# Kernel optimization log

Measured on AMD Instinct MI355X. Metric: run time of the kernel, lower is better.

Reference implementation:

```python
import jax, jax.numpy as jnp
import numpy as np

B, N, H = 16, 1024, 1024


def setup_inputs() -> dict:
    key = jax.random.key(0)
    ks = jax.random.split(key, 12)
    inv = 1.0 / np.sqrt(H)
    inp = {
        "x": jax.random.normal(ks[0], (B, N, H), jnp.float32),
        "atom_graph": jax.random.normal(ks[1], (B, N, N), jnp.float32),
        "variable_graph": jax.random.normal(ks[2], (B, N, N), jnp.float32),
        "Wq": jax.random.uniform(ks[3], (H, H), jnp.float32, -inv, inv),
        "bq": jax.random.uniform(ks[4], (H,), jnp.float32, -inv, inv),
        "Wk": jax.random.uniform(ks[5], (H, H), jnp.float32, -inv, inv),
        "bk": jax.random.uniform(ks[6], (H,), jnp.float32, -inv, inv),
        "Wv": jax.random.uniform(ks[7], (H, H), jnp.float32, -inv, inv),
        "bv": jax.random.uniform(ks[8], (H,), jnp.float32, -inv, inv),
        "predicate_pos": jax.random.randint(ks[9], (B, N), 0, 2, jnp.int32),
        "variable_tags": jax.random.randint(ks[10], (B, N), 0, 4, jnp.int32),
    }
    return inp


def _path_pool(h, predicate_pos):
    # h: [B,N,H]; predicate_pos: [B,N] in {0,1}
    b, n, d = h.shape
    i = jnp.arange(n)
    # pos[i-2] (value irrelevant for i<2, those branches handled explicitly)
    pp2 = jnp.pad(predicate_pos, ((0, 0), (2, 0)))[:, :n]  # [B,N]
    # window [s, e): i==0 -> [0,2); i==1 -> [0,3); pos[i-2]==1 -> [i,i+2); else [i-1,i+2)
    s = jnp.where(i < 2, 0, jnp.where(pp2 == 1, i, i - 1))  # [B,N]
    e = jnp.where(i == 0, 2, jnp.where(i == 1, 3, i + 2))    # [N]
    e = jnp.minimum(e, n)
    e = jnp.broadcast_to(e, (b, n))
    # prefix sums along node dim with a leading zero row -> windowed means via gather
    cs = jnp.concatenate([jnp.zeros((b, 1, d), h.dtype), jnp.cumsum(h, axis=1)], axis=1)  # [B,N+1,H]
    win_sum = (jnp.take_along_axis(cs, e[:, :, None], axis=1)
               - jnp.take_along_axis(cs, s[:, :, None], axis=1))  # [B,N,H]
    means = win_sum / (e - s)[:, :, None].astype(h.dtype)
    mask = (predicate_pos == 1).astype(h.dtype)  # [B,N]
    item = (means * mask[:, :, None]).sum(axis=1) / mask.sum(axis=1)[:, None]  # [B,H]
    return jnp.broadcast_to(item[:, None, :], (b, n, d))


def reference(x, atom_graph, variable_graph, Wq, bq, Wk, bk, Wv, bv,
              predicate_pos, variable_tags):
    scale = x.shape[-1] ** (-0.5)
    q = (x @ Wq.T + bq) * scale
    k = x @ Wk.T + bk
    v = x @ Wv.T + bv
    att = jnp.einsum("bnh,bmh->bnm", q, k) + atom_graph + variable_graph
    att = jax.nn.softmax(att, axis=-1)  # dropout is identity in eval
    h = jnp.einsum("bnm,bmh->bnh", att, v)
    return _path_pool(h, predicate_pos)
```

## Files before the change

### kernel.cpp

```cpp
#include <hip/hip_runtime.h>
#include <hip/hip_bf16.h>

#define BATCH 16
#define SEQ   1024
#define DIM   1024

typedef __attribute__((ext_vector_type(8))) short bf16x8;
typedef __attribute__((ext_vector_type(4))) float f32x4;
typedef __attribute__((ext_vector_type(4))) unsigned short us4;

__device__ __forceinline__ float bfu2f(unsigned short u) {
  union { unsigned int i; float f; } c; c.i = ((unsigned int)u) << 16; return c.f;
}
__device__ __forceinline__ unsigned short f2bfu(float f) {
  union { float f; unsigned int i; } c; c.f = f;
  return (unsigned short)((c.i + 0x7FFFu + ((c.i >> 16) & 1u)) >> 16);
}
__device__ __forceinline__ void async16(void* lds, const void* g) {
  __builtin_amdgcn_global_load_lds(
      (const __attribute__((address_space(1))) unsigned int*)g,
      (__attribute__((address_space(3))) unsigned int*)lds, 16, 0, 0);
}

__global__ void cast_xw_kernel(const float* __restrict__ x, const float* __restrict__ Wv,
                               unsigned short* __restrict__ xb,
                               unsigned short* __restrict__ Wvb, int x4) {
  int i = blockIdx.x * blockDim.x + threadIdx.x;
  const float* in; unsigned short* out; int j;
  if (i < x4) { in = x; out = xb; j = i; }
  else { in = Wv; out = Wvb; j = i - x4; }
  f32x4 v = ((const f32x4*)in)[j];
  us4 o;
  o[0] = f2bfu(v[0]); o[1] = f2bfu(v[1]); o[2] = f2bfu(v[2]); o[3] = f2bfu(v[3]);
  ((us4*)out)[j] = o;
}

__global__ void castT_kernel(const float* __restrict__ Wq, const float* __restrict__ Wk,
                             unsigned short* __restrict__ WqT,
                             unsigned short* __restrict__ WkT) {
  const float* in = (blockIdx.z == 0) ? Wq : Wk;
  unsigned short* out = (blockIdx.z == 0) ? WqT : WkT;
  __shared__ float t[64][65];
  const int h0 = blockIdx.x * 64, i0 = blockIdx.y * 64;
  const int tid = threadIdx.x;
  const int sub = tid >> 4, c4 = tid & 15;
#pragma unroll
  for (int p = 0; p < 4; ++p) {
    const int row = p * 16 + sub;
    f32x4 v = *(const f32x4*)(in + (size_t)(h0 + row) * DIM + i0 + c4 * 4);
    t[row][c4 * 4 + 0] = v[0]; t[row][c4 * 4 + 1] = v[1];
    t[row][c4 * 4 + 2] = v[2]; t[row][c4 * 4 + 3] = v[3];
  }
  __syncthreads();
#pragma unroll
  for (int p = 0; p < 4; ++p) {
    const int orow = p * 16 + sub;
    us4 o;
    o[0] = f2bfu(t[c4 * 4 + 0][orow]);
    o[1] = f2bfu(t[c4 * 4 + 1][orow]);
    o[2] = f2bfu(t[c4 * 4 + 2][orow]);
    o[3] = f2bfu(t[c4 * 4 + 3][orow]);
    *(us4*)(out + (size_t)(i0 + orow) * DIM + h0 + c4 * 4) = o;
  }
}

__global__ void t12_kernel(const unsigned short* __restrict__ WqT,
                           const unsigned short* __restrict__ WkT,
                           const float* __restrict__ bq, const float* __restrict__ bk,
                           float* __restrict__ t1, float* __restrict__ t2) {
  const int y = blockIdx.y;
  const unsigned short* Wt = y ? WkT : WqT;
  const float* vec = y ? bq : bk;
  float* tout = y ? t2 : t1;
  const int wave = threadIdx.x >> 6, lane = threadIdx.x & 63;
  const int i = blockIdx.x * 4 + wave;
  const us4* wr = (const us4*)(Wt + (size_t)i * DIM);
  float s = 0.f;
#pragma unroll
  for (int t = 0; t < 4; ++t) {
    us4 w4 = wr[lane + 64 * t];
    f32x4 b4 = *(const f32x4*)(vec + (lane + 64 * t) * 4);
    s += bfu2f(w4[0]) * b4[0] + bfu2f(w4[1]) * b4[1] +
         bfu2f(w4[2]) * b4[2] + bfu2f(w4[3]) * b4[3];
  }
#pragma unroll
  for (int o = 32; o; o >>= 1) s += __shfl_down(s, o);
  if (lane == 0) tout[i] = s;
}

__global__ void ac_kernel(const unsigned short* __restrict__ xb,
                          const float* __restrict__ t1, const float* __restrict__ t2,
                          const float* __restrict__ bq, const float* __restrict__ bk,
                          float* __restrict__ a, float* __restrict__ c) {
  const float scale = 0.03125f;
  const int tid = threadIdx.x;
  const int wave = tid >> 6, lane = tid & 63;
  float dp = 0.f;
  for (int i = tid; i < DIM; i += 256) dp += bq[i] * bk[i];
#pragma unroll
  for (int o = 32; o; o >>= 1) dp += __shfl_down(dp, o);
  __shared__ float dred[4];
  if ((tid & 63) == 0) dred[tid >> 6] = dp;
  __syncthreads();
  const float d = dred[0] + dred[1] + dred[2] + dred[3];
  float t1r[16], t2r[16];
#pragma unroll
  for (int t = 0; t < 4; ++t) {
    f32x4 v1 = *(const f32x4*)(t1 + (lane + 64 * t) * 4);
    f32x4 v2 = *(const f32x4*)(t2 + (lane + 64 * t) * 4);
#pragma unroll
    for (int j = 0; j < 4; ++j) { t1r[t * 4 + j] = v1[j]; t2r[t * 4 + j] = v2[j]; }
  }
  for (int rr = 0; rr < 16; ++rr) {
    const int row = blockIdx.x * 64 + wave * 16 + rr;
    const us4* xr = (const us4*)(xb + (size_t)row * DIM);
    float sa = 0.f, sc = 0.f;
#pragma unroll
    for (int t = 0; t < 4; ++t) {
      us4 v = xr[lane + 64 * t];
#pragma unroll
      for (int j = 0; j < 4; ++j) {
        const float f = bfu2f(v[j]);
        sa += f * t1r[t * 4 + j];
        sc += f * t2r[t * 4 + j];
      }
    }
#pragma unroll
    for (int o = 32; o; o >>= 1) { sa += __shfl_down(sa, o); sc += __shfl_down(sc, o); }
    if (lane == 0) {
      a[row] = scale * (sa + d);
      c[row] = scale * sc;
    }
  }
}

__global__ void pathw_kernel(const int* __restrict__ pos, float* __restrict__ w,
                             float* __restrict__ zbias) {
  const int b = blockIdx.x;
  __shared__ int ps[SEQ];
  __shared__ int mcnt;
  const int tid = threadIdx.x;
  if (tid == 0) mcnt = 0;
  __syncthreads();
  if (b == 0)
    for (int i = tid; i < DIM; i += 256) zbias[i] = 0.f;
  for (int i = tid; i < SEQ; i += 256) ps[i] = pos[b * SEQ + i];
  __syncthreads();
  int c = 0;
  for (int i = tid; i < SEQ; i += 256) c += ps[i];
  for (int o = 32; o; o >>= 1) c += __shfl_down(c, o);
  if ((tid & 63) == 0) atomicAdd(&mcnt, c);
  __syncthreads();
  const float invM = 1.0f / (float)mcnt;
  for (int j = tid; j < SEQ; j += 256) {
    float a = 0.f;
#pragma unroll
    for (int di = -1; di <= 1; ++di) {
      int i = j + di;
      if (i < 0 || i >= SEQ) continue;
      if (!ps[i]) continue;
      int s, e;
      if (i < 2) { s = 0; e = (i == 0) ? 2 : 3; }
      else { s = (ps[i - 2] == 1) ? i : (i - 1); e = i + 2; if (e > SEQ) e = SEQ; }
      if (s <= j && j < e) a += 1.0f / (float)(e - s);
    }
    w[b * SEQ + j] = a * invM;
  }
}

__global__ void proj_gemm(const unsigned short* __restrict__ A,
                          const unsigned short* __restrict__ W,
                          const float* __restrict__ bias, float alpha,
                          unsigned short* __restrict__ C, int M, int N, int K)
{
  __shared__ __align__(16) char smem[32768];
  float* Sl = (float*)smem;
  const int tid = threadIdx.x;
  const int wave = tid >> 6, lane = tid & 63;
  const int lr = lane & 15, lg = lane >> 4;
  const int wr = wave >> 1, wc = wave & 1;
  const int m0 = blockIdx.x * 128, n0 = blockIdx.y * 128;
  const int off0 = tid * 16, off1 = 4096 + tid * 16;
  const int r0 = off0 >> 6, ke0 = (off0 >> 1) & 31;
  const int r1 = off1 >> 6, ke1 = (off1 >> 1) & 31;
  f32x4 acc[4][4] = {};

  auto stage = [&](char* base, int kk) {
    async16(base + off0, A + (size_t)(m0 + r0) * K + kk + ke0);
    async16(base + off1, A + (size_t)(m0 + r1) * K + kk + ke1);
    async16(base + 8192 + off0, W + (size_t)(n0 + r0) * K + kk + ke0);
    async16(base + 8192 + off1, W + (size_t)(n0 + r1) * K + kk + ke1);
  };
  auto compute = [&](const char* base) {
    bf16x8 af[4], bfv[4];
#pragma unroll
    for (int i = 0; i < 4; ++i) {
      af[i]  = *(const bf16x8*)(base + ((wr * 64 + i * 16 + lr) << 6) + (lg << 4));
      bfv[i] = *(const bf16x8*)(base + 8192 + ((wc * 64 + i * 16 + lr) << 6) + (lg << 4));
    }
#pragma unroll
    for (int i = 0; i < 4; ++i)
#pragma unroll
      for (int j = 0; j < 4; ++j)
        acc[i][j] = __builtin_amdgcn_mfma_f32_16x16x32_bf16(af[i], bfv[j], acc[i][j], 0, 0, 0);
  };

  const int nt = K >> 5;
  stage(smem, 0);
  __syncthreads();
  int cur = 0;
  for (int k = 0; k < nt - 1; ++k) {
    stage(smem + ((cur ^ 1) << 14), (k + 1) << 5);
    compute(smem + (cur << 14));
    __syncthreads();
    cur ^= 1;
  }
  compute(smem + (cur << 14));
#pragma unroll
  for (int p = 0; p < 4; ++p) {
    __syncthreads();
    if (wr == (p >> 1)) {
      const int ibase = (p & 1) * 2;
#pragma unroll
      for (int ii = 0; ii < 2; ++ii) {
        const int i = ibase + ii;
#pragma unroll
        for (int j = 0; j < 4; ++j)
#pragma unroll
          for (int r = 0; r < 4; ++r)
            Sl[(ii * 16 + lg * 4 + r) * 132 + wc * 64 + j * 16 + lr] = acc[i][j][r];
      }
    }
    __syncthreads();
#pragma unroll
    for (int it = 0; it < 4; ++it) {
      const int v = tid + it * 256;
      const int lrow = v >> 5, c4 = v & 31;
      const int grow = m0 + p * 32 + lrow;
      const int col = n0 + c4 * 4;
      const f32x4 s4 = *(const f32x4*)(&Sl[lrow * 132 + c4 * 4]);
      const f32x4 b4 = *(const f32x4*)(bias + col);
      us4 o;
      o[0] = f2bfu((s4[0] + b4[0]) * alpha);
      o[1] = f2bfu((s4[1] + b4[1]) * alpha);
      o[2] = f2bfu((s4[2] + b4[2]) * alpha);
      o[3] = f2bfu((s4[3] + b4[3]) * alpha);
      *(us4*)(C + (size_t)grow * N + col) = o;
    }
  }
}

__global__ __launch_bounds__(512, 2)
void gemm256(const unsigned short* __restrict__ A,
             const unsigned short* __restrict__ B,
             unsigned short* __restrict__ C)
{
  extern __shared__ __align__(16) char smem[];
  const size_t boff = (size_t)blockIdx.z << 20;
  const int m0 = blockIdx.y * 256, n0 = blockIdx.x * 256;
  const int tid = threadIdx.x;
  const int lane = tid & 63;
  const int wid = tid >> 6;
  const int wm = wid >> 2, wn = wid & 3;
  const int lr = lane & 15, lg = lane >> 4;
  const unsigned short* Ab = A + boff;
  const unsigned short* Bb = B + boff;

  int sr[2], se[2], sL[2];
#pragma unroll
  for (int l = 0; l < 2; ++l) {
    const int L = l * 8192 + tid * 16;
    const int r = L >> 6, sp = (L >> 4) & 3;
    sL[l] = L; sr[l] = r; se[l] = (sp ^ ((r >> 1) & 3)) * 8;
  }
  int aoff[8], boff_[4];
#pragma unroll
  for (int i = 0; i < 8; ++i) {
    const int row = wm * 128 + i * 16 + lr;
    aoff[i] = row * 64 + (lg ^ ((row >> 1) & 3)) * 16;
  }
#pragma unroll
  for (int j = 0; j < 4; ++j) {
    const int row = wn * 64 + j * 16 + lr;
    boff_[j] = row * 64 + (lg ^ ((row >> 1) & 3)) * 16;
  }

  auto stage = [&](int slot, int kt) {
    char* sa = smem + slot * 32768;
#pragma unroll
    for (int l = 0; l < 2; ++l)
      async16(sa + sL[l], Ab + (size_t)(m0 + sr[l]) * DIM + kt * 32 + se[l]);
    char* sb = sa + 16384;
#pragma unroll
    for (int l = 0; l < 2; ++l)
      async16(sb + sL[l], Bb + (size_t)(n0 + sr[l]) * DIM + kt * 32 + se[l]);
  };

  f32x4 acc[8][4] = {};
  stage(0, 0); stage(1, 1); stage(2, 2); stage(3, 3);

#pragma unroll
  for (int t = 0; t < 32; ++t) {
    const int rem = 31 - t;
    if (rem >= 3)      asm volatile("s_waitcnt vmcnt(12)" ::: "memory");
    else if (rem == 2) asm volatile("s_waitcnt vmcnt(8)" ::: "memory");
    else if (rem == 1) asm volatile("s_waitcnt vmcnt(4)" ::: "memory");
    else               asm volatile("s_waitcnt vmcnt(0)" ::: "memory");
    __builtin_amdgcn_s_barrier();
    const char* sa = smem + (t & 3) * 32768;
    const char* sb = sa + 16384;
    bf16x8 a[8], bfr[4];
#pragma unroll
    for (int i = 0; i < 8; ++i) a[i] = *(const bf16x8*)(sa + aoff[i]);
#pragma unroll
    for (int j = 0; j < 4; ++j) bfr[j] = *(const bf16x8*)(sb + boff_[j]);
    __builtin_amdgcn_s_setprio(1);
#pragma unroll
    for (int i = 0; i < 8; ++i)
#pragma unroll
      for (int j = 0; j < 4; ++j)
        acc[i][j] = __builtin_amdgcn_mfma_f32_16x16x32_bf16(a[i], bfr[j], acc[i][j], 0, 0, 0);
    __builtin_amdgcn_s_setprio(0);
    __builtin_amdgcn_s_barrier();
    if (t + 4 < 32) stage(t & 3, t + 4);
  }

  unsigned short* Sl = (unsigned short*)smem;
  unsigned short* Cb = C + boff;
#pragma unroll
  for (int half = 0; half < 2; ++half) {
    __syncthreads();
    if (wm == half) {
#pragma unroll
      for (int i = 0; i < 8; ++i)
#pragma unroll
        for (int j = 0; j < 4; ++j)
#pragma unroll
          for (int r = 0; r < 4; ++r)
            Sl[(i * 16 + lg * 4 + r) * 260 + wn * 64 + j * 16 + lr] =
                f2bfu(acc[i][j][r]);
    }
    __syncthreads();
#pragma unroll
    for (int it = 0; it < 16; ++it) {
      const int v = tid + it * 512;
      const int row = v >> 6, c4 = v & 63;
      *(us4*)(Cb + (size_t)(m0 + half * 128 + row) * SEQ + n0 + c4 * 4) =
          *(const us4*)(&Sl[row * 260 + c4 * 4]);
    }
  }
}

__global__ void exp_fused_kernel(const unsigned short* __restrict__ S,
                                 const float* __restrict__ ag, const float* __restrict__ vg,
                                 const float* __restrict__ av, const float* __restrict__ cv,
                                 const float* __restrict__ w, float* __restrict__ part)
{
  __shared__ float red[4][SEQ];
  const int b = blockIdx.y;
  const int tid = threadIdx.x;
  const int wave = tid >> 6, lane = tid & 63;
  const float* agb = ag + ((size_t)b << 20);
  const float* vgb = vg + ((size_t)b << 20);
  const unsigned short* Sb = S + ((size_t)b << 20);
  const float* cvb = cv + b * SEQ;
  f32x4 cq[4];
#pragma unroll
  for (int qi = 0; qi < 4; ++qi)
    cq[qi] = *(const f32x4*)(cvb + (lane + 64 * qi) * 4);
  f32x4 ur[4] = {};
  const int r0 = blockIdx.x * 8 + wave * 2;
#pragma unroll
  for (int r = 0; r < 2; ++r) {
    const int row = r0 + r;
    const float wrow = w[b * SEQ + row];
    if (wrow == 0.f) continue;
    const float arow = av[b * SEQ + row];
    us4 sv[4]; f32x4 a4[4], g4[4];
#pragma unroll
    for (int qi = 0; qi < 4; ++qi) {
      const size_t base = (size_t)row * SEQ + (lane + 64 * qi) * 4;
      sv[qi] = *(const us4*)(Sb + base);
      a4[qi] = *(const f32x4*)(agb + base);
      g4[qi] = *(const f32x4*)(vgb + base);
    }
    float e[16];
    float rs = 0.f;
#pragma unroll
    for (int qi = 0; qi < 4; ++qi)
#pragma unroll
      for (int j = 0; j < 4; ++j) {
        const float ev = __expf(bfu2f(sv[qi][j]) + a4[qi][j] + g4[qi][j] + arow + cq[qi][j]);
        e[qi * 4 + j] = ev;
        rs += ev;
      }
#pragma unroll
    for (int o2 = 32; o2; o2 >>= 1) rs += __shfl_xor(rs, o2);
    const float cn = wrow / rs;
#pragma unroll
    for (int qi = 0; qi < 4; ++qi)
#pragma unroll
      for (int j = 0; j < 4; ++j)
        ur[qi][j] += cn * e[qi * 4 + j];
  }
#pragma unroll
  for (int qi = 0; qi < 4; ++qi)
    *(f32x4*)(&red[wave][(lane + 64 * qi) * 4]) = ur[qi];
  __syncthreads();
  const int col = tid * 4;
  f32x4 s0 = *(const f32x4*)(&red[0][col]);
  const f32x4 s1 = *(const f32x4*)(&red[1][col]);
  const f32x4 s2 = *(const f32x4*)(&red[2][col]);
  const f32x4 s3 = *(const f32x4*)(&red[3][col]);
  s0[0] += s1[0] + s2[0] + s3[0];
  s0[1] += s1[1] + s2[1] + s3[1];
  s0[2] += s1[2] + s2[2] + s3[2];
  s0[3] += s1[3] + s2[3] + s3[3];
  *(f32x4*)(part + ((size_t)(b * 128 + blockIdx.x) << 10) + col) = s0;
}

__global__ void wcol_kernel(const unsigned short* __restrict__ Mt,
                            const float* __restrict__ wv,
                            float* __restrict__ part) {
  const int nc = blockIdx.x;
  const int b = blockIdx.y;
  const int tid = threadIdx.x;
  __shared__ float c[64];
  if (tid < 64) c[tid] = wv[b * SEQ + nc * 64 + tid];
  __syncthreads();
  const unsigned short* p = Mt + ((size_t)b << 20) + ((size_t)(nc * 64) << 10) + tid * 4;
  f32x4 acc = {0.f, 0.f, 0.f, 0.f};
#pragma unroll 8
  for (int n = 0; n < 64; ++n) {
    const us4 v = *(const us4*)(p + ((size_t)n << 10));
    const float cn = c[n];
    acc[0] += cn * bfu2f(v[0]); acc[1] += cn * bfu2f(v[1]);
    acc[2] += cn * bfu2f(v[2]); acc[3] += cn * bfu2f(v[3]);
  }
  *(f32x4*)(part + (size_t)((b * 16 + nc) << 10) + tid * 4) = acc;
}

__global__ void wred_kernel(const float* __restrict__ part, float* __restrict__ vec,
                            int nchunks) {
  const int b = blockIdx.x;
  const int tid = threadIdx.x;
  f32x4 s = {0.f, 0.f, 0.f, 0.f};
  for (int nc = 0; nc < nchunks; ++nc) {
    const f32x4 v = *(const f32x4*)(part + ((size_t)(b * nchunks + nc) << 10) + tid * 4);
    s[0] += v[0]; s[1] += v[1]; s[2] += v[2]; s[3] += v[3];
  }
  *(f32x4*)(vec + b * SEQ + tid * 4) = s;
}

__global__ void item_kernel(const float* __restrict__ y,
                            const unsigned short* __restrict__ Wvb,
                            const float* __restrict__ bv, float* __restrict__ item) {
  const int b = blockIdx.x;
  const int hblk = blockIdx.y;
  __shared__ float ys[DIM];
  const int tid = threadIdx.x;
  for (int i = tid; i < DIM; i += 256) ys[i] = y[b * DIM + i];
  __syncthreads();
  const int wave = tid >> 6, lane = tid & 63;
  const int h = hblk * 4 + wave;
  const us4* wrow = (const us4*)(Wvb + (size_t)h * DIM);
  float acc = 0.f;
#pragma unroll
  for (int t = 0; t < 4; ++t) {
    us4 v = wrow[t * 64 + lane];
    const int d0 = (t * 64 + lane) * 4;
    acc += ys[d0] * bfu2f(v[0]) + ys[d0 + 1] * bfu2f(v[1]) +
           ys[d0 + 2] * bfu2f(v[2]) + ys[d0 + 3] * bfu2f(v[3]);
  }
  for (int o = 32; o; o >>= 1) acc += __shfl_down(acc, o);
  if (lane == 0) item[b * DIM + h] = acc + bv[h];
}

__global__ void bcast_kernel(const float* __restrict__ item, float* __restrict__ out) {
  const int b = blockIdx.y;
  const int n = blockIdx.x;
  const f32x4* src = (const f32x4*)(item + b * DIM);
  f32x4* dst = (f32x4*)(out + (((size_t)b * SEQ + n) << 10));
  dst[threadIdx.x] = src[threadIdx.x];
}

extern "C" void kernel_launch(void* const* d_in, const int* in_sizes, int n_in,
                              void* d_out, int out_size, void* d_ws, size_t ws_size,
                              hipStream_t stream) {
  const float* x    = (const float*)d_in[0];
  const float* ag   = (const float*)d_in[1];
  const float* vgr  = (const float*)d_in[2];
  const float* Wq   = (const float*)d_in[3];
  const float* bq   = (const float*)d_in[4];
  const float* Wk   = (const float*)d_in[5];
  const float* bk   = (const float*)d_in[6];
  const float* Wv   = (const float*)d_in[7];
  const float* bv   = (const float*)d_in[8];
  const int*   pos  = (const int*)d_in[9];
  float* out = (float*)d_out;

  char* ws = (char*)d_ws;
  size_t off = 0;
  auto alloc = [&](size_t bytes) { void* p = ws + off; off += (bytes + 255) & ~(size_t)255; return p; };
  const size_t BNH = (size_t)BATCH * SEQ * DIM;
  unsigned short* xb   = (unsigned short*)alloc(BNH * 2);
  unsigned short* zb   = (unsigned short*)alloc(BNH * 2);
  unsigned short* S    = (unsigned short*)alloc(BNH * 2);
  unsigned short* WqT  = (unsigned short*)alloc((size_t)DIM * DIM * 2);
  unsigned short* WkT  = (unsigned short*)alloc((size_t)DIM * DIM * 2);
  unsigned short* Wvb  = (unsigned short*)alloc((size_t)DIM * DIM * 2);
  unsigned short* Hb   = (unsigned short*)alloc((size_t)DIM * DIM * 2);
  float* w     = (float*)alloc((size_t)BATCH * SEQ * 4);
  float* u     = (float*)alloc((size_t)BATCH * SEQ * 4);
  float* av    = (float*)alloc((size_t)BATCH * SEQ * 4);
  float* cvv   = (float*)alloc((size_t)BATCH * SEQ * 4);
  float* t1    = (float*)alloc((size_t)DIM * 4);
  float* t2    = (float*)alloc((size_t)DIM * 4);
  float* zbias = (float*)alloc((size_t)DIM * 4);
  float* y     = (float*)alloc((size_t)BATCH * DIM * 4);
  float* item  = (float*)alloc((size_t)BATCH * DIM * 4);
  float* part  = (float*)alloc((size_t)BATCH * 128 * SEQ * 4);

  const float scale = 0.03125f;
  const int x4 = (int)(BNH / 4);

  (void)hipFuncSetAttribute(reinterpret_cast<const void*>(gemm256),
                            hipFuncAttributeMaxDynamicSharedMemorySize, 131072);

  cast_xw_kernel<<<(x4 + DIM * DIM / 4) / 256, 256, 0, stream>>>(x, Wv, xb, Wvb, x4);
  castT_kernel<<<dim3(16, 16, 2), 256, 0, stream>>>(Wq, Wk, WqT, WkT);

  pathw_kernel<<<BATCH, 256, 0, stream>>>(pos, w, zbias);

  t12_kernel<<<dim3(256, 2), 256, 0, stream>>>(WqT, WkT, bq, bk, t1, t2);
  ac_kernel<<<256, 256, 0, stream>>>(xb, t1, t2, bq, bk, av, cvv);

  proj_gemm<<<dim3(8, 8), 256, 0, stream>>>(WkT, WqT, zbias, scale, Hb, DIM, DIM, DIM);

  gemm256<<<dim3(4, 64, 1), 512, 131072, stream>>>(xb, Hb, zb);

  gemm256<<<dim3(4, 4, BATCH), 512, 131072, stream>>>(zb, xb, S);

  exp_fused_kernel<<<dim3(128, BATCH), 256, 0, stream>>>(S, ag, vgr, av, cvv, w, part);
  wred_kernel<<<BATCH, 256, 0, stream>>>(part, u, 128);

  wcol_kernel<<<dim3(16, BATCH), 256, 0, stream>>>(xb, u, part);
  wred_kernel<<<BATCH, 256, 0, stream>>>(part, y, 16);

  item_kernel<<<dim3(BATCH, 256), 256, 0, stream>>>(y, Wvb, bv, item);

  bcast_kernel<<<dim3(SEQ, BATCH), 256, 0, stream>>>(item, out);
}
```

Measured before the change: 239.2 us.

## Double-buffer GEMM LDS fragments, batch exp loads, fuse partial reduction into wcol

The GEMM main loop now reads the next stage's LDS fragments into a second register set before issuing MFMAs on the current one, so LDS reads overlap matrix math. The exp kernel issues the global loads for both rows before computing either, which raises memory-level parallelism. The separate wred pass over the 128 partial sums is removed; each wcol block reduces the partials it needs itself, saving a launch at the cost of redundant partial reads. Register pressure in the GEMM rises because fragment storage doubles.

```diff
diff --git a/kernel.cpp b/kernel.cpp
--- a/kernel.cpp
+++ b/kernel.cpp
@@ -296,30 +296,39 @@
       async16(sb + sL[l], Bb + (size_t)(n0 + sr[l]) * DIM + kt * 32 + se[l]);
   };
 
+  bf16x8 afr[2][8], bfr2[2][4];
+  auto readfrag = [&](int par, int slot) {
+    const char* sa = smem + slot * 32768;
+    const char* sb = sa + 16384;
+#pragma unroll
+    for (int i = 0; i < 8; ++i) afr[par][i] = *(const bf16x8*)(sa + aoff[i]);
+#pragma unroll
+    for (int j = 0; j < 4; ++j) bfr2[par][j] = *(const bf16x8*)(sb + boff_[j]);
+  };
+
   f32x4 acc[8][4] = {};
   stage(0, 0); stage(1, 1); stage(2, 2); stage(3, 3);
+  asm volatile("s_waitcnt vmcnt(12)" ::: "memory");
+  __builtin_amdgcn_s_barrier();
+  readfrag(0, 0);
 
 #pragma unroll
   for (int t = 0; t < 32; ++t) {
-    const int rem = 31 - t;
-    if (rem >= 3)      asm volatile("s_waitcnt vmcnt(12)" ::: "memory");
-    else if (rem == 2) asm volatile("s_waitcnt vmcnt(8)" ::: "memory");
-    else if (rem == 1) asm volatile("s_waitcnt vmcnt(4)" ::: "memory");
-    else               asm volatile("s_waitcnt vmcnt(0)" ::: "memory");
-    __builtin_amdgcn_s_barrier();
-    const char* sa = smem + (t & 3) * 32768;
-    const char* sb = sa + 16384;
-    bf16x8 a[8], bfr[4];
-#pragma unroll
-    for (int i = 0; i < 8; ++i) a[i] = *(const bf16x8*)(sa + aoff[i]);
-#pragma unroll
-    for (int j = 0; j < 4; ++j) bfr[j] = *(const bf16x8*)(sb + boff_[j]);
+    if (t < 31) {
+      if (t <= 28)      asm volatile("s_waitcnt vmcnt(8)" ::: "memory");
+      else if (t == 29) asm volatile("s_waitcnt vmcnt(4)" ::: "memory");
+      else              asm volatile("s_waitcnt vmcnt(0)" ::: "memory");
+      __builtin_amdgcn_s_barrier();
+      readfrag((t + 1) & 1, (t + 1) & 3);
+    }
+    const int par = t & 1;
     __builtin_amdgcn_s_setprio(1);
 #pragma unroll
     for (int i = 0; i < 8; ++i)
 #pragma unroll
       for (int j = 0; j < 4; ++j)
-        acc[i][j] = __builtin_amdgcn_mfma_f32_16x16x32_bf16(a[i], bfr[j], acc[i][j], 0, 0, 0);
+        acc[i][j] = __builtin_amdgcn_mfma_f32_16x16x32_bf16(afr[par][i], bfr2[par][j],
+                                                            acc[i][j], 0, 0, 0);
     __builtin_amdgcn_s_setprio(0);
     __builtin_amdgcn_s_barrier();
     if (t + 4 < 32) stage(t & 3, t + 4);
@@ -370,33 +379,42 @@
     cq[qi] = *(const f32x4*)(cvb + (lane + 64 * qi) * 4);
   f32x4 ur[4] = {};
   const int r0 = blockIdx.x * 8 + wave * 2;
+  const float w0 = w[b * SEQ + r0];
+  const float w1 = w[b * SEQ + r0 + 1];
+  us4 sv[2][4]; f32x4 a4[2][4], g4[2][4];
 #pragma unroll
   for (int r = 0; r < 2; ++r) {
+    const float wr_ = r ? w1 : w0;
+    if (wr_ == 0.f) continue;
     const int row = r0 + r;
-    const float wrow = w[b * SEQ + row];
-    if (wrow == 0.f) continue;
-    const float arow = av[b * SEQ + row];
-    us4 sv[4]; f32x4 a4[4], g4[4];
 #pragma unroll
     for (int qi = 0; qi < 4; ++qi) {
       const size_t base = (size_t)row * SEQ + (lane + 64 * qi) * 4;
-      sv[qi] = *(const us4*)(Sb + base);
-      a4[qi] = *(const f32x4*)(agb + base);
-      g4[qi] = *(const f32x4*)(vgb + base);
-    }
+      sv[r][qi] = *(const us4*)(Sb + base);
+      a4[r][qi] = *(const f32x4*)(agb + base);
+      g4[r][qi] = *(const f32x4*)(vgb + base);
+    }
+  }
+#pragma unroll
+  for (int r = 0; r < 2; ++r) {
+    const float wr_ = r ? w1 : w0;
+    if (wr_ == 0.f) continue;
+    const int row = r0 + r;
+    const float arow = av[b * SEQ + row];
     float e[16];
     float rs = 0.f;
 #pragma unroll
     for (int qi = 0; qi < 4; ++qi)
 #pragma unroll
       for (int j = 0; j < 4; ++j) {
-        const float ev = __expf(bfu2f(sv[qi][j]) + a4[qi][j] + g4[qi][j] + arow + cq[qi][j]);
+        const float ev = __expf(bfu2f(sv[r][qi][j]) + a4[r][qi][j] + g4[r][qi][j] +
+                                arow + cq[qi][j]);
         e[qi * 4 + j] = ev;
         rs += ev;
       }
 #pragma unroll
     for (int o2 = 32; o2; o2 >>= 1) rs += __shfl_xor(rs, o2);
-    const float cn = wrow / rs;
+    const float cn = wr_ / rs;
 #pragma unroll
     for (int qi = 0; qi < 4; ++qi)
 #pragma unroll
@@ -421,12 +439,29 @@
 
 __global__ void wcol_kernel(const unsigned short* __restrict__ Mt,
                             const float* __restrict__ wv,
+                            const float* __restrict__ pin,
                             float* __restrict__ part) {
   const int nc = blockIdx.x;
   const int b = blockIdx.y;
   const int tid = threadIdx.x;
   __shared__ float c[64];
-  if (tid < 64) c[tid] = wv[b * SEQ + nc * 64 + tid];
+  if (pin) {
+    const int n = nc * 64 + (tid & 63);
+    const int bl0 = (tid >> 6) * 32;
+    float s = 0.f;
+#pragma unroll 8
+    for (int bl = 0; bl < 32; ++bl)
+      s += pin[((size_t)(b * 128 + bl0 + bl) << 10) + n];
+#pragma unroll
+    for (int o = 32; o; o >>= 1) {
+    }
+    __shared__ float cp[4][64];
+    cp[tid >> 6][tid & 63] = s;
+    __syncthreads();
+    if (tid < 64) c[tid] = cp[0][tid] + cp[1][tid] + cp[2][tid] + cp[3][tid];
+  } else {
+    if (tid < 64) c[tid] = wv[b * SEQ + nc * 64 + tid];
+  }
   __syncthreads();
   const unsigned short* p = Mt + ((size_t)b << 20) + ((size_t)(nc * 64) << 10) + tid * 4;
   f32x4 acc = {0.f, 0.f, 0.f, 0.f};
@@ -511,7 +546,6 @@
   unsigned short* Wvb  = (unsigned short*)alloc((size_t)DIM * DIM * 2);
   unsigned short* Hb   = (unsigned short*)alloc((size_t)DIM * DIM * 2);
   float* w     = (float*)alloc((size_t)BATCH * SEQ * 4);
-  float* u     = (float*)alloc((size_t)BATCH * SEQ * 4);
   float* av    = (float*)alloc((size_t)BATCH * SEQ * 4);
   float* cvv   = (float*)alloc((size_t)BATCH * SEQ * 4);
   float* t1    = (float*)alloc((size_t)DIM * 4);
@@ -519,7 +553,8 @@
   float* zbias = (float*)alloc((size_t)DIM * 4);
   float* y     = (float*)alloc((size_t)BATCH * DIM * 4);
   float* item  = (float*)alloc((size_t)BATCH * DIM * 4);
-  float* part  = (float*)alloc((size_t)BATCH * 128 * SEQ * 4);
+  float* partU = (float*)alloc((size_t)BATCH * 128 * SEQ * 4);
+  float* partY = (float*)alloc((size_t)BATCH * 16 * SEQ * 4);
 
   const float scale = 0.03125f;
   const int x4 = (int)(BNH / 4);
@@ -541,11 +576,10 @@
 
   gemm256<<<dim3(4, 4, BATCH), 512, 131072, stream>>>(zb, xb, S);
 
-  exp_fused_kernel<<<dim3(128, BATCH), 256, 0, stream>>>(S, ag, vgr, av, cvv, w, part);
-  wred_kernel<<<BATCH, 256, 0, stream>>>(part, u, 128);
-
-  wcol_kernel<<<dim3(16, BATCH), 256, 0, stream>>>(xb, u, part);
-  wred_kernel<<<BATCH, 256, 0, stream>>>(part, y, 16);
+  exp_fused_kernel<<<dim3(128, BATCH), 256, 0, stream>>>(S, ag, vgr, av, cvv, w, partU);
+
+  wcol_kernel<<<dim3(16, BATCH), 256, 0, stream>>>(xb, nullptr, partU, partY);
+  wred_kernel<<<BATCH, 256, 0, stream>>>(partY, y, 16);
 
   item_kernel<<<dim3(BATCH, 256), 256, 0, stream>>>(y, Wvb, bv, item);
 
```

New measurement: 260.8 us. 1.09x slower.
